# Performance work log

Measured on AMD Instinct MI355X. Metric: run time of the kernel, lower is better.

## Reference

```python
import jax, jax.numpy as jnp
import numpy as np

HEADS = 16


def setup_inputs() -> dict:
    key = jax.random.key(0)
    k1, k2, k3 = jax.random.split(key, 3)
    B, T, D = 2, 2048, 1024
    x = jax.random.normal(k1, (B, T, D), dtype=jnp.float32)
    # causal mask, broadcast over batch and heads
    mask = jnp.tril(jnp.ones((T, T), dtype=bool))[None, None, :, :]
    # torch Linear(dim, 3*dim, bias=False): weight [3D, D]; we store transposed [D, 3D]
    Wqkv = jax.random.normal(k2, (D, 3 * D), dtype=jnp.float32) * (D ** -0.5)
    Wo = jax.random.normal(k3, (D, D), dtype=jnp.float32) * (D ** -0.5)
    return {"x": x, "mask": mask, "Wqkv": Wqkv, "Wo": Wo}


def reference(x, mask, Wqkv, Wo):
    B, T, D = x.shape
    h = HEADS
    dh = D // h
    scale = dh ** -0.5
    qkv = (x @ Wqkv).reshape(B, T, 3, h, dh)
    qkv = jnp.transpose(qkv, (2, 0, 3, 1, 4))  # [3, B, h, T, dh]
    q, k, v = qkv[0], qkv[1], qkv[2]
    att = jnp.einsum("bhqd,bhkd->bhqk", q, k) * scale  # [B, h, T, T]
    att = jnp.where(mask, att, jnp.float32(-1e9))
    att = jax.nn.softmax(att, axis=-1)
    # dropout: identity in eval/reference mode
    out = jnp.einsum("bhqk,bhkd->bhqd", att, v)  # [B, h, T, dh]
    out = jnp.transpose(out, (0, 2, 1, 3)).reshape(B, T, D)
    return out @ Wo
```

## Files before the change

kernel.cpp:

```cpp
#include <hip/hip_runtime.h>
#include <cstdint>

typedef unsigned short ushort_t;
typedef __attribute__((ext_vector_type(8))) short short8;
typedef __attribute__((ext_vector_type(4))) float f32x4;

#define B_ 2
#define T_ 2048
#define D_ 1024
#define H_ 16
#define DH_ 64

__device__ inline unsigned short f2bf(float f) {
  unsigned int u = __float_as_uint(f);
  u += 0x7FFF + ((u >> 16) & 1);
  return (unsigned short)(u >> 16);
}

__device__ inline unsigned short f2bf_fast(float f) {
  return (unsigned short)((__float_as_uint(f) + 0x8000u) >> 16);
}

__device__ inline f32x4 mfma16(short8 a, short8 b, f32x4 c) {
  return __builtin_amdgcn_mfma_f32_16x16x32_bf16(a, b, c, 0, 0, 0);
}

__device__ inline void gload16(const void* g, void* l) {
  __builtin_amdgcn_global_load_lds(
      (const __attribute__((address_space(1))) unsigned int*)(uintptr_t)g,
      (__attribute__((address_space(3))) unsigned int*)(uint32_t)(uintptr_t)l,
      16, 0, 0);
}

__global__ void k_cvt(const float* __restrict__ in, ushort_t* __restrict__ out, int n4) {
  int i = blockIdx.x * blockDim.x + threadIdx.x;
  if (i >= n4) return;
  float4 v = ((const float4*)in)[i];
  ushort4 o;
  o.x = f2bf(v.x); o.y = f2bf(v.y); o.z = f2bf(v.z); o.w = f2bf(v.w);
  ((ushort4*)out)[i] = o;
}

__global__ void k_tcvt(const float* __restrict__ in, ushort_t* __restrict__ out,
                       int R, int C) {
  __shared__ float tile[32][33];
  int c0 = blockIdx.x * 32, r0 = blockIdx.y * 32;
  int tx = threadIdx.x, ty = threadIdx.y;
#pragma unroll
  for (int i = 0; i < 32; i += 8)
    tile[ty + i][tx] = in[(size_t)(r0 + ty + i) * C + c0 + tx];
  __syncthreads();
#pragma unroll
  for (int i = 0; i < 32; i += 8)
    out[(size_t)(c0 + ty + i) * R + r0 + tx] = f2bf(tile[tx][ty + i]);
}

__global__ void k_pack_qk(const ushort_t* __restrict__ qkv,
                          ushort_t* __restrict__ pq, ushort_t* __restrict__ pk) {
  const int t16 = blockIdx.x, bh = blockIdx.y;
  const int b = bh >> 4, hh = bh & 15;
  const int tsel = threadIdx.x >> 6;
  const int l = threadIdx.x & 63;
  const int lrow = l & 15, lg = l >> 4;
  ushort_t* dst = (tsel ? pk : pq) + (size_t)(bh * 128 + t16) * 1024 + l * 8;
  const ushort_t* src = qkv + (size_t)(b * T_ + t16 * 16 + lrow) * (3 * D_)
                        + tsel * D_ + hh * DH_ + lg * 8;
  short8 v0 = *(const short8*)(src);
  short8 v1 = *(const short8*)(src + 32);
  if (tsel == 0) {
    const float SC = 0.125f * 1.44269504f;
#pragma unroll
    for (int i = 0; i < 8; ++i) {
      float f0 = __uint_as_float(((unsigned)(unsigned short)v0[i]) << 16) * SC;
      float f1 = __uint_as_float(((unsigned)(unsigned short)v1[i]) << 16) * SC;
      v0[i] = (short)f2bf(f0);
      v1[i] = (short)f2bf(f1);
    }
  }
  *(short8*)(dst)       = v0;
  *(short8*)(dst + 512) = v1;
}

__global__ void k_pack_v(const ushort_t* __restrict__ qkv, ushort_t* __restrict__ pv) {
  __shared__ ushort_t tile[32][68];
  const int t32 = blockIdx.x, bh = blockIdx.y;
  const int b = bh >> 4, hh = bh & 15;
  const int t = threadIdx.x;
  {
    const int row = t >> 3, ch = t & 7;
    *(short8*)&tile[row][ch * 8] =
        *(const short8*)(qkv + (size_t)(b * T_ + t32 * 32 + row) * (3 * D_)
                         + 2 * D_ + hh * DH_ + ch * 8);
  }
  __syncthreads();
  const int nt = t >> 6, l = t & 63;
  const int lrow = l & 15, lg = l >> 4;
  const int d = nt * 16 + lrow;
  short8 o;
#pragma unroll
  for (int i = 0; i < 8; ++i) o[i] = (short)tile[lg * 8 + i][d];
  *(short8*)(pv + ((size_t)(bh * 64 + t32) * 4 + nt) * 512 + l * 8) = o;
}

template <int OUTF>
__global__ __launch_bounds__(256, 2) void k_gemm_bt(
    const ushort_t* __restrict__ A, const ushort_t* __restrict__ Bt,
    void* __restrict__ C, int M, int N, int K) {
  __shared__ __align__(16) ushort_t As[128 * 32];
  __shared__ __align__(16) ushort_t Bs[128 * 32];
  const int tid = threadIdx.x;
  const int w = tid >> 6, l = tid & 63;
  const int bm = blockIdx.y, bn = blockIdx.x;
  const int wm = w >> 1, wn = w & 1;

  const f32x4 fz = {0.f, 0.f, 0.f, 0.f};
  f32x4 acc[4][4];
#pragma unroll
  for (int i = 0; i < 4; ++i)
#pragma unroll
    for (int j = 0; j < 4; ++j) acc[i][j] = fz;

  const int r_a = l >> 2;
  const int cb = (l & 3) * 16;
  const int lrow = l & 15;
  const int lk16 = (l >> 4) * 16;

  for (int k0 = 0; k0 < K; k0 += 32) {
    __syncthreads();
#pragma unroll
    for (int c = 0; c < 2; ++c) {
      int row = (w * 2 + c) * 16 + r_a;
      gload16((const char*)A + ((size_t)(bm * 128 + row) * K + k0) * 2 + cb,
              (char*)As + row * 64 + cb);
      gload16((const char*)Bt + ((size_t)(bn * 128 + row) * K + k0) * 2 + cb,
              (char*)Bs + row * 64 + cb);
    }
    __syncthreads();
    short8 af[4], bv[4];
#pragma unroll
    for (int mt = 0; mt < 4; ++mt)
      af[mt] = *(const short8*)((const char*)As + (wm * 64 + mt * 16 + lrow) * 64 + lk16);
#pragma unroll
    for (int nt = 0; nt < 4; ++nt)
      bv[nt] = *(const short8*)((const char*)Bs + (wn * 64 + nt * 16 + lrow) * 64 + lk16);
#pragma unroll
    for (int mt = 0; mt < 4; ++mt)
#pragma unroll
      for (int nt = 0; nt < 4; ++nt)
        acc[mt][nt] = mfma16(af[mt], bv[nt], acc[mt][nt]);
  }

  const int rg = (l >> 4) * 4;
#pragma unroll
  for (int mt = 0; mt < 4; ++mt)
#pragma unroll
    for (int nt = 0; nt < 4; ++nt) {
      size_t col = (size_t)bn * 128 + wn * 64 + nt * 16 + lrow;
#pragma unroll
      for (int r = 0; r < 4; ++r) {
        size_t rowi = (size_t)bm * 128 + wm * 64 + mt * 16 + rg + r;
        if (OUTF)
          ((float*)C)[rowi * N + col] = acc[mt][nt][r];
        else
          ((ushort_t*)C)[rowi * N + col] = f2bf(acc[mt][nt][r]);
      }
    }
}

__global__ __launch_bounds__(128) void k_attn(
    const ushort_t* __restrict__ pq, const ushort_t* __restrict__ pk,
    const ushort_t* __restrict__ pv, ushort_t* __restrict__ ctx) {
  __shared__ __align__(16) ushort_t plds[2][2][16][72];
  const int tid = threadIdx.x;
  const int w = tid >> 6, l = tid & 63;
  const int n = blockIdx.x;
  const int q = n >> 3;
  const int bh = (n & 7) * 4 + (q & 3);
  const int j2 = (31 - (q >> 2)) * 2 + w;
  const int b = bh >> 4, hh = bh & 15;
  const int jlo = j2 * 2;
  const int qr0 = jlo * 16;
  const int lrow = l & 15, lg = l >> 4;

  const ushort_t* pqb = pq + (size_t)(bh * 128 + jlo) * 1024 + l * 8;
  short8 aq00 = *(const short8*)(pqb);
  short8 aq01 = *(const short8*)(pqb + 512);
  short8 aq10 = *(const short8*)(pqb + 1024);
  short8 aq11 = *(const short8*)(pqb + 1536);

  const f32x4 fz = {0.f, 0.f, 0.f, 0.f};
  f32x4 o0[4], o1[4];
#pragma unroll
  for (int nt = 0; nt < 4; ++nt) { o0[nt] = fz; o1[nt] = fz; }
  float ls0[4] = {0.f, 0.f, 0.f, 0.f};
  float ls1[4] = {0.f, 0.f, 0.f, 0.f};

  const int ntiles = (j2 >> 1) + 1;
  for (int t = 0; t < ntiles; ++t) {
    const int kv0 = t * 64;
    const ushort_t* pkb = pk + (size_t)(bh * 128 + (kv0 >> 4)) * 1024 + l * 8;
    short8 bk0[4], bk1[4];
#pragma unroll
    for (int nh = 0; nh < 4; ++nh) {
      bk0[nh] = *(const short8*)(pkb + nh * 1024);
      bk1[nh] = *(const short8*)(pkb + nh * 1024 + 512);
    }
    f32x4 s0[4], s1[4];
    __builtin_amdgcn_s_setprio(1);
#pragma unroll
    for (int nh = 0; nh < 4; ++nh) {
      s0[nh] = mfma16(aq01, bk1[nh], mfma16(aq00, bk0[nh], fz));
      s1[nh] = mfma16(aq11, bk1[nh], mfma16(aq10, bk0[nh], fz));
    }
    __builtin_amdgcn_s_setprio(0);
    if (t == ntiles - 1) {
#pragma unroll
      for (int r = 0; r < 4; ++r) {
        int row0 = qr0 + lg * 4 + r;
#pragma unroll
        for (int nh = 0; nh < 4; ++nh) {
          int col = kv0 + nh * 16 + lrow;
          if (col > row0)      s0[nh][r] = -1e30f;
          if (col > row0 + 16) s1[nh][r] = -1e30f;
        }
      }
    }
    const ushort_t* pvb = pv + (size_t)(bh * 64 + (kv0 >> 5)) * 2048 + l * 8;
    short8 bv0[4], bv1[4];
#pragma unroll
    for (int nt = 0; nt < 4; ++nt) {
      bv0[nt] = *(const short8*)(pvb + nt * 512);
      bv1[nt] = *(const short8*)(pvb + 2048 + nt * 512);
    }
#pragma unroll
    for (int r = 0; r < 4; ++r) {
      float a0 = __builtin_amdgcn_exp2f(s0[0][r]);
      float a1 = __builtin_amdgcn_exp2f(s0[1][r]);
      float a2 = __builtin_amdgcn_exp2f(s0[2][r]);
      float a3 = __builtin_amdgcn_exp2f(s0[3][r]);
      float c0 = __builtin_amdgcn_exp2f(s1[0][r]);
      float c1 = __builtin_amdgcn_exp2f(s1[1][r]);
      float c2 = __builtin_amdgcn_exp2f(s1[2][r]);
      float c3 = __builtin_amdgcn_exp2f(s1[3][r]);
      ls0[r] += (a0 + a1) + (a2 + a3);
      ls1[r] += (c0 + c1) + (c2 + c3);
      plds[w][0][lg * 4 + r][lrow]      = f2bf_fast(a0);
      plds[w][0][lg * 4 + r][16 + lrow] = f2bf_fast(a1);
      plds[w][0][lg * 4 + r][32 + lrow] = f2bf_fast(a2);
      plds[w][0][lg * 4 + r][48 + lrow] = f2bf_fast(a3);
      plds[w][1][lg * 4 + r][lrow]      = f2bf_fast(c0);
      plds[w][1][lg * 4 + r][16 + lrow] = f2bf_fast(c1);
      plds[w][1][lg * 4 + r][32 + lrow] = f2bf_fast(c2);
      plds[w][1][lg * 4 + r][48 + lrow] = f2bf_fast(c3);
    }
    short8 pa00 = *(const short8*)&plds[w][0][lrow][lg * 8];
    short8 pa01 = *(const short8*)&plds[w][0][lrow][32 + lg * 8];
    short8 pa10 = *(const short8*)&plds[w][1][lrow][lg * 8];
    short8 pa11 = *(const short8*)&plds[w][1][lrow][32 + lg * 8];
    __builtin_amdgcn_s_setprio(1);
#pragma unroll
    for (int nt = 0; nt < 4; ++nt) {
      o0[nt] = mfma16(pa01, bv1[nt], mfma16(pa00, bv0[nt], o0[nt]));
      o1[nt] = mfma16(pa11, bv1[nt], mfma16(pa10, bv0[nt], o1[nt]));
    }
    __builtin_amdgcn_s_setprio(0);
  }
#pragma unroll
  for (int r = 0; r < 4; ++r) {
#pragma unroll
    for (int x = 1; x < 16; x <<= 1) {
      ls0[r] += __shfl_xor(ls0[r], x);
      ls1[r] += __shfl_xor(ls1[r], x);
    }
  }
#pragma unroll
  for (int nt = 0; nt < 4; ++nt) {
#pragma unroll
    for (int r = 0; r < 4; ++r) {
      int row0 = qr0 + lg * 4 + r;
      size_t base = (size_t)b * T_ + row0;
      ctx[(base) * D_ + hh * DH_ + nt * 16 + lrow] =
          f2bf(o0[nt][r] / ls0[r]);
      ctx[(base + 16) * D_ + hh * DH_ + nt * 16 + lrow] =
          f2bf(o1[nt][r] / ls1[r]);
    }
  }
}

extern "C" void kernel_launch(void* const* d_in, const int* in_sizes, int n_in,
                              void* d_out, int out_size, void* d_ws, size_t ws_size,
                              hipStream_t stream) {
  const float* x    = (const float*)d_in[0];
  const float* Wqkv = (const float*)d_in[2];
  const float* Wo   = (const float*)d_in[3];
  float* out = (float*)d_out;

  char* ws = (char*)d_ws;
  ushort_t* xb    = (ushort_t*)(ws);
  ushort_t* wqkvT = (ushort_t*)(ws + (8u  << 20));
  ushort_t* woT   = (ushort_t*)(ws + (14u << 20));
  ushort_t* qkvb  = (ushort_t*)(ws + (16u << 20));
  ushort_t* pq    = (ushort_t*)(ws + (40u << 20));
  ushort_t* pk    = (ushort_t*)(ws + (48u << 20));
  ushort_t* pv    = (ushort_t*)(ws);
  ushort_t* ctxb  = (ushort_t*)(ws + (16u << 20));

  dim3 tb(32, 8);
  k_cvt<<<(B_ * T_ * D_) / 4 / 256, 256, 0, stream>>>(x, xb, (B_ * T_ * D_) / 4);
  k_tcvt<<<dim3(96, 32), tb, 0, stream>>>(Wqkv, wqkvT, 1024, 3072);
  k_tcvt<<<dim3(32, 32), tb, 0, stream>>>(Wo, woT, 1024, 1024);
  k_gemm_bt<0><<<dim3(24, 32), 256, 0, stream>>>(xb, wqkvT, qkvb, 4096, 3072, 1024);
  k_pack_qk<<<dim3(128, 32), 128, 0, stream>>>(qkvb, pq, pk);
  k_pack_v<<<dim3(64, 32), 256, 0, stream>>>(qkvb, pv);
  k_attn<<<1024, 128, 0, stream>>>(pq, pk, pv, ctxb);
  k_gemm_bt<1><<<dim3(8, 32), 256, 0, stream>>>(ctxb, woT, out, 4096, 1024, 1024);
}
```

Measured before the change: 204.3 us.

## Fuse QKV packing into GEMM epilogue and use single-wave attention blocks

The QKV projection GEMM now writes Q (pre-scaled), K and V directly into the MFMA-packed layouts the attention kernel expects. This removes the intermediate qkv buffer and the two pack kernels, along with their extra global read and write passes. The epilogue writes are scattered 2-byte stores, so they may coalesce poorly. Attention also moves from 128-thread blocks with two waves to 64-thread single-wave blocks with twice as many blocks, which changes per-block LDS use and how work is scheduled.

Measured after the change: 195.7 us. 4.2% less time.

```diff
diff --git a/kernel.cpp b/kernel.cpp
--- a/kernel.cpp
+++ b/kernel.cpp
@@ -55,51 +55,85 @@
     out[(size_t)(c0 + ty + i) * R + r0 + tx] = f2bf(tile[tx][ty + i]);
 }
 
-__global__ void k_pack_qk(const ushort_t* __restrict__ qkv,
-                          ushort_t* __restrict__ pq, ushort_t* __restrict__ pk) {
-  const int t16 = blockIdx.x, bh = blockIdx.y;
-  const int b = bh >> 4, hh = bh & 15;
-  const int tsel = threadIdx.x >> 6;
-  const int l = threadIdx.x & 63;
-  const int lrow = l & 15, lg = l >> 4;
-  ushort_t* dst = (tsel ? pk : pq) + (size_t)(bh * 128 + t16) * 1024 + l * 8;
-  const ushort_t* src = qkv + (size_t)(b * T_ + t16 * 16 + lrow) * (3 * D_)
-                        + tsel * D_ + hh * DH_ + lg * 8;
-  short8 v0 = *(const short8*)(src);
-  short8 v1 = *(const short8*)(src + 32);
-  if (tsel == 0) {
-    const float SC = 0.125f * 1.44269504f;
-#pragma unroll
-    for (int i = 0; i < 8; ++i) {
-      float f0 = __uint_as_float(((unsigned)(unsigned short)v0[i]) << 16) * SC;
-      float f1 = __uint_as_float(((unsigned)(unsigned short)v1[i]) << 16) * SC;
-      v0[i] = (short)f2bf(f0);
-      v1[i] = (short)f2bf(f1);
-    }
-  }
-  *(short8*)(dst)       = v0;
-  *(short8*)(dst + 512) = v1;
-}
-
-__global__ void k_pack_v(const ushort_t* __restrict__ qkv, ushort_t* __restrict__ pv) {
-  __shared__ ushort_t tile[32][68];
-  const int t32 = blockIdx.x, bh = blockIdx.y;
-  const int b = bh >> 4, hh = bh & 15;
-  const int t = threadIdx.x;
-  {
-    const int row = t >> 3, ch = t & 7;
-    *(short8*)&tile[row][ch * 8] =
-        *(const short8*)(qkv + (size_t)(b * T_ + t32 * 32 + row) * (3 * D_)
-                         + 2 * D_ + hh * DH_ + ch * 8);
-  }
-  __syncthreads();
-  const int nt = t >> 6, l = t & 63;
-  const int lrow = l & 15, lg = l >> 4;
-  const int d = nt * 16 + lrow;
-  short8 o;
-#pragma unroll
-  for (int i = 0; i < 8; ++i) o[i] = (short)tile[lg * 8 + i][d];
-  *(short8*)(pv + ((size_t)(bh * 64 + t32) * 4 + nt) * 512 + l * 8) = o;
+__global__ __launch_bounds__(256, 2) void k_gemm_qkv(
+    const ushort_t* __restrict__ A, const ushort_t* __restrict__ Bt,
+    ushort_t* __restrict__ pq, ushort_t* __restrict__ pk,
+    ushort_t* __restrict__ pv) {
+  const int K = 1024, Kb = 2 * K;
+  __shared__ __align__(16) ushort_t As[128 * 32];
+  __shared__ __align__(16) ushort_t Bs[128 * 32];
+  const int tid = threadIdx.x;
+  const int w = tid >> 6, l = tid & 63;
+  const int bm = blockIdx.y, bn = blockIdx.x;
+  const int wm = w >> 1, wn = w & 1;
+
+  const f32x4 fz = {0.f, 0.f, 0.f, 0.f};
+  f32x4 acc[4][4];
+#pragma unroll
+  for (int i = 0; i < 4; ++i)
+#pragma unroll
+    for (int j = 0; j < 4; ++j) acc[i][j] = fz;
+
+  const int r_a = l >> 2;
+  const int cb = (l & 3) * 16;
+  const int lrow = l & 15;
+  const int lk16 = (l >> 4) * 16;
+
+  for (int k0 = 0; k0 < K; k0 += 32) {
+    __syncthreads();
+#pragma unroll
+    for (int c = 0; c < 2; ++c) {
+      int row = (w * 2 + c) * 16 + r_a;
+      gload16((const char*)A + (size_t)(bm * 128 + row) * Kb + k0 * 2 + cb,
+              (char*)As + row * 64 + cb);
+      gload16((const char*)Bt + (size_t)(bn * 128 + row) * Kb + k0 * 2 + cb,
+              (char*)Bs + row * 64 + cb);
+    }
+    __syncthreads();
+    short8 af[4], bv[4];
+#pragma unroll
+    for (int mt = 0; mt < 4; ++mt)
+      af[mt] = *(const short8*)((const char*)As + (wm * 64 + mt * 16 + lrow) * 64 + lk16);
+#pragma unroll
+    for (int nt = 0; nt < 4; ++nt)
+      bv[nt] = *(const short8*)((const char*)Bs + (wn * 64 + nt * 16 + lrow) * 64 + lk16);
+#pragma unroll
+    for (int mt = 0; mt < 4; ++mt)
+#pragma unroll
+      for (int nt = 0; nt < 4; ++nt)
+        acc[mt][nt] = mfma16(af[mt], bv[nt], acc[mt][nt]);
+  }
+
+  const int rg = (l >> 4) * 4;
+  const int s = bn >> 3;
+  const float QS = 0.125f * 1.44269504f;
+#pragma unroll
+  for (int mt = 0; mt < 4; ++mt)
+#pragma unroll
+    for (int nt = 0; nt < 4; ++nt) {
+      int gcol = bn * 128 + wn * 64 + nt * 16 + lrow;
+      int dh = gcol & 63, hh = (gcol >> 6) & 15;
+#pragma unroll
+      for (int r = 0; r < 4; ++r) {
+        int grow = bm * 128 + wm * 64 + mt * 16 + rg + r;
+        int b = grow >> 11, trow = grow & 2047;
+        int bh = b * 16 + hh;
+        float v = acc[mt][nt][r];
+        if (s == 0) v *= QS;
+        unsigned short u = f2bf(v);
+        if (s < 2) {
+          ushort_t* base = s ? pk : pq;
+          size_t off = (size_t)bh * (128 * 1024) + (size_t)(trow >> 4) * 1024 +
+                       (size_t)(dh >> 5) * 512 +
+                       (((trow & 15) + ((dh >> 3) & 3) * 16) << 3) + (dh & 7);
+          base[off] = (ushort_t)u;
+        } else {
+          size_t off = ((size_t)(bh * 64 + (trow >> 5)) * 4 + (dh >> 4)) * 512 +
+                       (((dh & 15) + ((trow >> 3) & 3) * 16) << 3) + (trow & 7);
+          pv[off] = (ushort_t)u;
+        }
+      }
+    }
 }
 
 template <int OUTF>
@@ -167,16 +201,15 @@
     }
 }
 
-__global__ __launch_bounds__(128) void k_attn(
+__global__ __launch_bounds__(64) void k_attn(
     const ushort_t* __restrict__ pq, const ushort_t* __restrict__ pk,
     const ushort_t* __restrict__ pv, ushort_t* __restrict__ ctx) {
-  __shared__ __align__(16) ushort_t plds[2][2][16][72];
-  const int tid = threadIdx.x;
-  const int w = tid >> 6, l = tid & 63;
+  __shared__ __align__(16) ushort_t plds[2][16][72];
+  const int l = threadIdx.x;
   const int n = blockIdx.x;
   const int q = n >> 3;
   const int bh = (n & 7) * 4 + (q & 3);
-  const int j2 = (31 - (q >> 2)) * 2 + w;
+  const int j2 = 63 - (q >> 2);
   const int b = bh >> 4, hh = bh & 15;
   const int jlo = j2 * 2;
   const int qr0 = jlo * 16;
@@ -244,19 +277,19 @@
       float c3 = __builtin_amdgcn_exp2f(s1[3][r]);
       ls0[r] += (a0 + a1) + (a2 + a3);
       ls1[r] += (c0 + c1) + (c2 + c3);
-      plds[w][0][lg * 4 + r][lrow]      = f2bf_fast(a0);
-      plds[w][0][lg * 4 + r][16 + lrow] = f2bf_fast(a1);
-      plds[w][0][lg * 4 + r][32 + lrow] = f2bf_fast(a2);
-      plds[w][0][lg * 4 + r][48 + lrow] = f2bf_fast(a3);
-      plds[w][1][lg * 4 + r][lrow]      = f2bf_fast(c0);
-      plds[w][1][lg * 4 + r][16 + lrow] = f2bf_fast(c1);
-      plds[w][1][lg * 4 + r][32 + lrow] = f2bf_fast(c2);
-      plds[w][1][lg * 4 + r][48 + lrow] = f2bf_fast(c3);
-    }
-    short8 pa00 = *(const short8*)&plds[w][0][lrow][lg * 8];
-    short8 pa01 = *(const short8*)&plds[w][0][lrow][32 + lg * 8];
-    short8 pa10 = *(const short8*)&plds[w][1][lrow][lg * 8];
-    short8 pa11 = *(const short8*)&plds[w][1][lrow][32 + lg * 8];
+      plds[0][lg * 4 + r][lrow]      = f2bf_fast(a0);
+      plds[0][lg * 4 + r][16 + lrow] = f2bf_fast(a1);
+      plds[0][lg * 4 + r][32 + lrow] = f2bf_fast(a2);
+      plds[0][lg * 4 + r][48 + lrow] = f2bf_fast(a3);
+      plds[1][lg * 4 + r][lrow]      = f2bf_fast(c0);
+      plds[1][lg * 4 + r][16 + lrow] = f2bf_fast(c1);
+      plds[1][lg * 4 + r][32 + lrow] = f2bf_fast(c2);
+      plds[1][lg * 4 + r][48 + lrow] = f2bf_fast(c3);
+    }
+    short8 pa00 = *(const short8*)&plds[0][lrow][lg * 8];
+    short8 pa01 = *(const short8*)&plds[0][lrow][32 + lg * 8];
+    short8 pa10 = *(const short8*)&plds[1][lrow][lg * 8];
+    short8 pa11 = *(const short8*)&plds[1][lrow][32 + lg * 8];
     __builtin_amdgcn_s_setprio(1);
 #pragma unroll
     for (int nt = 0; nt < 4; ++nt) {
@@ -299,19 +332,16 @@
   ushort_t* xb    = (ushort_t*)(ws);
   ushort_t* wqkvT = (ushort_t*)(ws + (8u  << 20));
   ushort_t* woT   = (ushort_t*)(ws + (14u << 20));
-  ushort_t* qkvb  = (ushort_t*)(ws + (16u << 20));
-  ushort_t* pq    = (ushort_t*)(ws + (40u << 20));
-  ushort_t* pk    = (ushort_t*)(ws + (48u << 20));
-  ushort_t* pv    = (ushort_t*)(ws);
-  ushort_t* ctxb  = (ushort_t*)(ws + (16u << 20));
+  ushort_t* pq    = (ushort_t*)(ws + (16u << 20));
+  ushort_t* pk    = (ushort_t*)(ws + (24u << 20));
+  ushort_t* pv    = (ushort_t*)(ws + (32u << 20));
+  ushort_t* ctxb  = (ushort_t*)(ws + (40u << 20));
 
   dim3 tb(32, 8);
   k_cvt<<<(B_ * T_ * D_) / 4 / 256, 256, 0, stream>>>(x, xb, (B_ * T_ * D_) / 4);
   k_tcvt<<<dim3(96, 32), tb, 0, stream>>>(Wqkv, wqkvT, 1024, 3072);
   k_tcvt<<<dim3(32, 32), tb, 0, stream>>>(Wo, woT, 1024, 1024);
-  k_gemm_bt<0><<<dim3(24, 32), 256, 0, stream>>>(xb, wqkvT, qkvb, 4096, 3072, 1024);
-  k_pack_qk<<<dim3(128, 32), 128, 0, stream>>>(qkvb, pq, pk);
-  k_pack_v<<<dim3(64, 32), 256, 0, stream>>>(qkvb, pv);
-  k_attn<<<1024, 128, 0, stream>>>(pq, pk, pv, ctxb);
+  k_gemm_qkv<<<dim3(24, 32), 256, 0, stream>>>(xb, wqkvT, pq, pk, pv);
+  k_attn<<<2048, 64, 0, stream>>>(pq, pk, pv, ctxb);
   k_gemm_bt<1><<<dim3(8, 32), 256, 0, stream>>>(ctxb, woT, out, 4096, 1024, 1024);
 }
```
